# Kernel optimization log

Hardware: AMD Instinct MI355X
Metric: run time of the kernel (lower is better)

The kernel has to match this reference:

```python
import jax, jax.numpy as jnp
import numpy as np

N_EMBED = 384
N_HEADS = 8
HEAD_SIZE = N_EMBED // N_HEADS  # 48
BLOCK = 64
LN_EPS = 1e-5


def _layernorm(x, g, b):
    mu = jnp.mean(x, axis=-1, keepdims=True)
    var = jnp.var(x, axis=-1, keepdims=True)
    return (x - mu) * jax.lax.rsqrt(var + LN_EPS) * g + b


def setup_inputs() -> dict:
    key = jax.random.key(0)
    ks = jax.random.split(key, 16)
    s = 0.02
    x = jax.random.normal(ks[0], (2048, BLOCK, N_EMBED), dtype=jnp.float32)
    # per-head Q/K/V linears, stacked over heads (equivalent to the 8 separate nn.Linear's)
    wq = jax.random.normal(ks[1], (N_HEADS, N_EMBED, HEAD_SIZE), dtype=jnp.float32) * s
    bq = jnp.zeros((N_HEADS, HEAD_SIZE), dtype=jnp.float32)
    wk = jax.random.normal(ks[2], (N_HEADS, N_EMBED, HEAD_SIZE), dtype=jnp.float32) * s
    bk = jnp.zeros((N_HEADS, HEAD_SIZE), dtype=jnp.float32)
    wv = jax.random.normal(ks[3], (N_HEADS, N_EMBED, HEAD_SIZE), dtype=jnp.float32) * s
    bv = jnp.zeros((N_HEADS, HEAD_SIZE), dtype=jnp.float32)
    wo = jax.random.normal(ks[4], (N_EMBED, N_EMBED), dtype=jnp.float32) * s
    bo = jnp.zeros((N_EMBED,), dtype=jnp.float32)
    w1 = jax.random.normal(ks[5], (N_EMBED, 4 * N_EMBED), dtype=jnp.float32) * s
    b1 = jnp.zeros((4 * N_EMBED,), dtype=jnp.float32)
    w2 = jax.random.normal(ks[6], (4 * N_EMBED, N_EMBED), dtype=jnp.float32) * s
    b2 = jnp.zeros((N_EMBED,), dtype=jnp.float32)
    g1 = jnp.ones((N_EMBED,), dtype=jnp.float32)
    be1 = jnp.zeros((N_EMBED,), dtype=jnp.float32)
    g2 = jnp.ones((N_EMBED,), dtype=jnp.float32)
    be2 = jnp.zeros((N_EMBED,), dtype=jnp.float32)
    return dict(x=x, wq=wq, bq=bq, wk=wk, bk=bk, wv=wv, bv=bv, wo=wo, bo=bo,
                w1=w1, b1=b1, w2=w2, b2=b2, g1=g1, be1=be1, g2=g2, be2=be2)


def reference(x, wq, bq, wk, bk, wv, bv, wo, bo, w1, b1, w2, b2, g1, be1, g2, be2):
    B, T, D = x.shape  # T == BLOCK
    # x = norm1(x)
    h = _layernorm(x, g1, be1)
    # multi-head causal attention (heads stacked; same math as 8 separate SelfAttention modules)
    q = jnp.einsum('btd,hde->bhte', h, wq) + bq[None, :, None, :]
    k = jnp.einsum('btd,hde->bhte', h, wk) + bk[None, :, None, :]
    v = jnp.einsum('btd,hde->bhte', h, wv) + bv[None, :, None, :]
    scores = jnp.einsum('bhte,bhse->bhts', q, k) * (HEAD_SIZE ** -0.5)
    causal = jnp.tril(jnp.ones((T, T), dtype=bool))
    scores = jnp.where(causal, scores, -jnp.inf)
    probs = jax.nn.softmax(scores, axis=-1)  # dropout is identity in eval
    attn = jnp.einsum('bhts,bhse->bhte', probs, v)
    attn = attn.transpose(0, 2, 1, 3).reshape(B, T, N_HEADS * HEAD_SIZE)  # concat heads
    attn = attn @ wo + bo
    # x = x + attn(x)  (residual from the normed x, per the original code)
    h = h + attn
    # x = norm2(x); x = x + ff(x)
    h2 = _layernorm(h, g2, be2)
    ff = jax.nn.relu(h2 @ w1 + b1) @ w2 + b2
    return h2 + ff
```

## Files before the change

kernel.cpp:

```cpp
#include <hip/hip_runtime.h>

typedef __attribute__((ext_vector_type(8))) short short8;
typedef __attribute__((ext_vector_type(4))) float f32x4;

#define LNE 1e-5f

__device__ __forceinline__ unsigned short f2bf(float f) {
  union { float f; unsigned int u; } v; v.f = f;
  unsigned int r = v.u + 0x7fffu + ((v.u >> 16) & 1u);
  return (unsigned short)(r >> 16);
}
__device__ __forceinline__ float bf2f(unsigned short s) {
  union { unsigned int u; float f; } v; v.u = ((unsigned int)s) << 16;
  return v.f;
}
__device__ __forceinline__ unsigned int pk2(float a, float b) {
  return (unsigned int)f2bf(a) | ((unsigned int)f2bf(b) << 16);
}
__device__ __forceinline__ short8 ld8(const unsigned short* p, int k) {
  return *(const short8*)(p + k * 32);
}

__global__ void prep_kernel(const float* __restrict__ wq, const float* __restrict__ wk,
                            const float* __restrict__ wv, const float* __restrict__ wo,
                            const float* __restrict__ w1, const float* __restrict__ w2,
                            unsigned short* __restrict__ ws) {
  int idx = blockIdx.x * 256 + threadIdx.x;
  if (idx < 442368) {
    int n = idx / 384, d = idx % 384;
    int mat = n / 384, rem = n % 384, head = rem / 48, e = rem % 48;
    const float* w = (mat == 0) ? wq : ((mat == 1) ? wk : wv);
    ws[idx] = f2bf(w[(head * 384 + d) * 48 + e]);
  } else if (idx < 589824) {
    int j = idx - 442368; int n = j / 384, d = j % 384;
    ws[idx] = f2bf(wo[d * 384 + n]);
  } else if (idx < 1179648) {
    int j = idx - 589824; int n = j / 384, d = j % 384;
    ws[idx] = f2bf(w1[d * 1536 + n]);
  } else if (idx < 1769472) {
    int j = idx - 1179648; int n = j / 1536, c = j % 1536;
    ws[idx] = f2bf(w2[c * 384 + n]);
  }
}

__global__ __launch_bounds__(512, 2) void block_fused(
    const float* __restrict__ x,
    const float* __restrict__ bq, const float* __restrict__ bk, const float* __restrict__ bv,
    const float* __restrict__ bo, const float* __restrict__ b1, const float* __restrict__ b2,
    const float* __restrict__ g1, const float* __restrict__ be1,
    const float* __restrict__ g2, const float* __restrict__ be2,
    const unsigned short* __restrict__ wt,
    float* __restrict__ out) {
  __shared__ __align__(16) unsigned short sH[64 * 392];
  __shared__ __align__(16) unsigned short sA[64 * 392];
  __shared__ __align__(16) unsigned short sS[25344];

  const int tid  = threadIdx.x;
  const int wave = tid >> 6, lane = tid & 63;
  const int quad = lane >> 4, l15 = lane & 15;
  const int g = wave >> 2, w4 = wave & 3;
  const int b = blockIdx.x;

  const unsigned short* wqkvT = wt;
  const unsigned short* woT   = wt + 442368;
  const unsigned short* w1T   = wt + 589824;
  const unsigned short* w2T   = wt + 1179648;

  unsigned short* sQg = sS + g * 4608;
  unsigned short* sKg = sS + 9216 + g * 4608;
  unsigned short* sVg = sS + 18432 + g * 3456;

  {
    {
      int set = tid >> 8, j = tid & 255;
      int r = j >> 2, cc = 48 + (j & 3) * 4;
      *(uint2*)&sS[set * 4608 + r * 72 + cc] = make_uint2(0, 0);
      *(uint2*)&sS[9216 + set * 4608 + r * 72 + cc] = make_uint2(0, 0);
    }
    const int r = tid >> 3, sub = tid & 7;
    const float* xr = x + ((size_t)b * 64 + r) * 384 + sub * 48;
    float s = 0.f, s2 = 0.f;
#pragma unroll
    for (int i = 0; i < 12; ++i) {
      float4 v = ((const float4*)xr)[i];
      s  += v.x + v.y + v.z + v.w;
      s2 += v.x * v.x + v.y * v.y + v.z * v.z + v.w * v.w;
    }
    s  += __shfl_xor(s, 1);  s  += __shfl_xor(s, 2);  s  += __shfl_xor(s, 4);
    s2 += __shfl_xor(s2, 1); s2 += __shfl_xor(s2, 2); s2 += __shfl_xor(s2, 4);
    float mu = s * (1.f / 384.f);
    float rstd = rsqrtf(s2 * (1.f / 384.f) - mu * mu + LNE);
#pragma unroll
    for (int i = 0; i < 12; ++i) {
      float4 v = ((const float4*)xr)[i];
      int c = sub * 48 + i * 4;
      float h0 = (v.x - mu) * rstd * g1[c + 0] + be1[c + 0];
      float h1 = (v.y - mu) * rstd * g1[c + 1] + be1[c + 1];
      float h2 = (v.z - mu) * rstd * g1[c + 2] + be1[c + 2];
      float h3 = (v.w - mu) * rstd * g1[c + 3] + be1[c + 3];
      *(uint2*)&sH[r * 392 + c] = make_uint2(pk2(h0, h1), pk2(h2, h3));
    }
  }
  __syncthreads();

#pragma unroll 1
  for (int hp = 0; hp < 4; ++hp) {
    const int h = hp * 2 + g;
    if (hp) {
      int set = tid >> 8, j = tid & 255;
      int r = j >> 2, cc = 48 + (j & 3) * 4;
      *(uint2*)&sS[set * 4608 + r * 72 + cc] = make_uint2(0, 0);
    }
    {
      const int s0m = w4 / 3, s0e = w4 % 3;
      const int s1m = (w4 + 4) / 3, s1e = (w4 + 4) % 3;
      const bool has2 = (w4 == g);
      const unsigned short* bp0 = wqkvT + ((size_t)(s0m * 8 + h) * 48 + s0e * 16 + l15) * 384 + quad * 8;
      const unsigned short* bp1 = wqkvT + ((size_t)(s1m * 8 + h) * 48 + s1e * 16 + l15) * 384 + quad * 8;
      const unsigned short* bp2 = wqkvT + ((size_t)(16 + h) * 48 + 32 + l15) * 384 + quad * 8;
      const unsigned short* abase = sH + l15 * 392 + quad * 8;

      f32x4 acc0[4], acc1[4], acc2[4];
#pragma unroll
      for (int mt = 0; mt < 4; ++mt) {
        acc0[mt] = (f32x4){0.f, 0.f, 0.f, 0.f};
        acc1[mt] = (f32x4){0.f, 0.f, 0.f, 0.f};
        acc2[mt] = (f32x4){0.f, 0.f, 0.f, 0.f};
      }
      short8 b0[4], b1[4], b2[4];
#pragma unroll
      for (int k = 0; k < 3; ++k) {
        b0[k] = ld8(bp0, k); b1[k] = ld8(bp1, k);
        if (has2) b2[k] = ld8(bp2, k);
      }
#pragma unroll
      for (int k = 0; k < 12; ++k) {
        if (k < 9) {
          int sl = (k + 3) & 3;
          b0[sl] = ld8(bp0, k + 3); b1[sl] = ld8(bp1, k + 3);
          if (has2) b2[sl] = ld8(bp2, k + 3);
        }
        short8 a[4];
#pragma unroll
        for (int mt = 0; mt < 4; ++mt) a[mt] = *(const short8*)(abase + mt * 16 * 392 + k * 32);
        int sl = k & 3;
#pragma unroll
        for (int mt = 0; mt < 4; ++mt)
          acc0[mt] = __builtin_amdgcn_mfma_f32_16x16x32_bf16(a[mt], b0[sl], acc0[mt], 0, 0, 0);
#pragma unroll
        for (int mt = 0; mt < 4; ++mt)
          acc1[mt] = __builtin_amdgcn_mfma_f32_16x16x32_bf16(a[mt], b1[sl], acc1[mt], 0, 0, 0);
        if (has2) {
#pragma unroll
          for (int mt = 0; mt < 4; ++mt)
            acc2[mt] = __builtin_amdgcn_mfma_f32_16x16x32_bf16(a[mt], b2[sl], acc2[mt], 0, 0, 0);
        }
      }
      auto wrQKV = [&](int mat, int et, f32x4* acc) {
        const float* bias = (mat == 0) ? bq : ((mat == 1) ? bk : bv);
        float bsv = bias[h * 48 + et * 16 + l15];
        if (mat == 2) {
#pragma unroll
          for (int mt = 0; mt < 4; ++mt)
            *(uint2*)&sVg[(et * 16 + l15) * 72 + mt * 16 + quad * 4] =
                make_uint2(pk2(acc[mt][0] + bsv, acc[mt][1] + bsv),
                           pk2(acc[mt][2] + bsv, acc[mt][3] + bsv));
        } else {
          unsigned short* dst = (mat == 0) ? sQg : sKg;
#pragma unroll
          for (int mt = 0; mt < 4; ++mt)
#pragma unroll
            for (int i = 0; i < 4; ++i)
              dst[(mt * 16 + quad * 4 + i) * 72 + et * 16 + l15] = f2bf(acc[mt][i] + bsv);
        }
      };
      wrQKV(s0m, s0e, acc0);
      wrQKV(s1m, s1e, acc1);
      if (has2) wrQKV(2, 2, acc2);
    }
    __syncthreads();

    f32x4 sc[4];
#pragma unroll
    for (int ts = 0; ts < 4; ++ts) {
      f32x4 acc = {0.f, 0.f, 0.f, 0.f};
#pragma unroll
      for (int k = 0; k < 2; ++k) {
        short8 a  = *(const short8*)&sQg[(w4 * 16 + l15) * 72 + k * 32 + quad * 8];
        short8 bb = *(const short8*)&sKg[(ts * 16 + l15) * 72 + k * 32 + quad * 8];
        acc = __builtin_amdgcn_mfma_f32_16x16x32_bf16(a, bb, acc, 0, 0, 0);
      }
      sc[ts] = acc;
    }
    const float scale = 0.14433756729740645f;
#pragma unroll
    for (int i = 0; i < 4; ++i) {
      int t = w4 * 16 + quad * 4 + i;
      float vv[4];
#pragma unroll
      for (int ts = 0; ts < 4; ++ts) {
        int s_ = ts * 16 + l15;
        float v = sc[ts][i] * scale;
        vv[ts] = (s_ <= t) ? v : -INFINITY;
      }
      float mx = fmaxf(fmaxf(vv[0], vv[1]), fmaxf(vv[2], vv[3]));
      mx = fmaxf(mx, __shfl_xor(mx, 1)); mx = fmaxf(mx, __shfl_xor(mx, 2));
      mx = fmaxf(mx, __shfl_xor(mx, 4)); mx = fmaxf(mx, __shfl_xor(mx, 8));
      float sum = 0.f;
#pragma unroll
      for (int ts = 0; ts < 4; ++ts) { vv[ts] = __expf(vv[ts] - mx); sum += vv[ts]; }
      sum += __shfl_xor(sum, 1); sum += __shfl_xor(sum, 2);
      sum += __shfl_xor(sum, 4); sum += __shfl_xor(sum, 8);
      float inv = 1.f / sum;
#pragma unroll
      for (int ts = 0; ts < 4; ++ts)
        sQg[t * 72 + ts * 16 + l15] = f2bf(vv[ts] * inv);
    }
#pragma unroll
    for (int et = 0; et < 3; ++et) {
      f32x4 acc = {0.f, 0.f, 0.f, 0.f};
#pragma unroll
      for (int k = 0; k < 2; ++k) {
        short8 a  = *(const short8*)&sVg[(et * 16 + l15) * 72 + k * 32 + quad * 8];
        short8 bb = *(const short8*)&sQg[(w4 * 16 + l15) * 72 + k * 32 + quad * 8];
        acc = __builtin_amdgcn_mfma_f32_16x16x32_bf16(a, bb, acc, 0, 0, 0);
      }
      *(uint2*)&sA[(w4 * 16 + l15) * 392 + h * 48 + et * 16 + quad * 4] =
          make_uint2(pk2(acc[0], acc[1]), pk2(acc[2], acc[3]));
    }
    __syncthreads();
  }

  {
    float* sRedS  = (float*)sS;
    float* sRedS2 = (float*)sS + 512;
    const unsigned short* bp[3];
#pragma unroll
    for (int nl = 0; nl < 3; ++nl)
      bp[nl] = woT + (size_t)((wave * 3 + nl) * 16 + l15) * 384 + quad * 8;
    f32x4 oacc[3][4];
#pragma unroll
    for (int nl = 0; nl < 3; ++nl)
#pragma unroll
      for (int mt = 0; mt < 4; ++mt) oacc[nl][mt] = (f32x4){0.f, 0.f, 0.f, 0.f};
    short8 bb[3][4];
#pragma unroll
    for (int k = 0; k < 3; ++k)
#pragma unroll
      for (int nl = 0; nl < 3; ++nl) bb[nl][k] = ld8(bp[nl], k);
#pragma unroll
    for (int k = 0; k < 12; ++k) {
      if (k < 9) {
        int sl = (k + 3) & 3;
#pragma unroll
        for (int nl = 0; nl < 3; ++nl) bb[nl][sl] = ld8(bp[nl], k + 3);
      }
      short8 a[4];
#pragma unroll
      for (int mt = 0; mt < 4; ++mt)
        a[mt] = *(const short8*)&sA[(mt * 16 + l15) * 392 + k * 32 + quad * 8];
      int sl = k & 3;
#pragma unroll
      for (int nl = 0; nl < 3; ++nl)
#pragma unroll
        for (int mt = 0; mt < 4; ++mt)
          oacc[nl][mt] = __builtin_amdgcn_mfma_f32_16x16x32_bf16(a[mt], bb[nl][sl], oacc[nl][mt], 0, 0, 0);
    }
#pragma unroll
    for (int nl = 0; nl < 3; ++nl) {
      int n = (wave * 3 + nl) * 16 + l15;
      float bov = bo[n];
#pragma unroll
      for (int mt = 0; mt < 4; ++mt)
#pragma unroll
        for (int i = 0; i < 4; ++i)
          oacc[nl][mt][i] += bov + bf2f(sH[(mt * 16 + quad * 4 + i) * 392 + n]);
    }
#pragma unroll
    for (int mt = 0; mt < 4; ++mt)
#pragma unroll
      for (int i = 0; i < 4; ++i) {
        float s = oacc[0][mt][i] + oacc[1][mt][i] + oacc[2][mt][i];
        float s2 = oacc[0][mt][i] * oacc[0][mt][i] + oacc[1][mt][i] * oacc[1][mt][i]
                 + oacc[2][mt][i] * oacc[2][mt][i];
        s  += __shfl_xor(s, 1);  s  += __shfl_xor(s, 2);  s  += __shfl_xor(s, 4);  s  += __shfl_xor(s, 8);
        s2 += __shfl_xor(s2, 1); s2 += __shfl_xor(s2, 2); s2 += __shfl_xor(s2, 4); s2 += __shfl_xor(s2, 8);
        if (l15 == 0) {
          int row = mt * 16 + quad * 4 + i;
          sRedS[row * 8 + wave] = s;
          sRedS2[row * 8 + wave] = s2;
        }
      }
    __syncthreads();
    float mu_[4][4], rs_[4][4];
#pragma unroll
    for (int mt = 0; mt < 4; ++mt)
#pragma unroll
      for (int i = 0; i < 4; ++i) {
        int row = mt * 16 + quad * 4 + i;
        float4 p0 = *(float4*)&sRedS[row * 8], p1 = *(float4*)&sRedS[row * 8 + 4];
        float4 q0 = *(float4*)&sRedS2[row * 8], q1 = *(float4*)&sRedS2[row * 8 + 4];
        float st  = p0.x + p0.y + p0.z + p0.w + p1.x + p1.y + p1.z + p1.w;
        float s2t = q0.x + q0.y + q0.z + q0.w + q1.x + q1.y + q1.z + q1.w;
        float mu = st * (1.f / 384.f);
        mu_[mt][i] = mu;
        rs_[mt][i] = rsqrtf(s2t * (1.f / 384.f) - mu * mu + LNE);
      }
#pragma unroll
    for (int nl = 0; nl < 3; ++nl) {
      int n = (wave * 3 + nl) * 16 + l15;
      float gv = g2[n], bev = be2[n];
#pragma unroll
      for (int mt = 0; mt < 4; ++mt)
#pragma unroll
        for (int i = 0; i < 4; ++i) {
          float h2v = (oacc[nl][mt][i] - mu_[mt][i]) * rs_[mt][i] * gv + bev;
          sH[(mt * 16 + quad * 4 + i) * 392 + n] = f2bf(h2v);
        }
    }
  }
  __syncthreads();

  f32x4 facc[4][3];
#pragma unroll
  for (int mt = 0; mt < 4; ++mt)
#pragma unroll
    for (int nl = 0; nl < 3; ++nl) facc[mt][nl] = (f32x4){0.f, 0.f, 0.f, 0.f};

  auto FFN1 = [&](int c, unsigned short* U) {
    const unsigned short* ap[3];
#pragma unroll
    for (int ml = 0; ml < 3; ++ml)
      ap[ml] = w1T + (size_t)(c * 384 + (wave * 3 + ml) * 16 + l15) * 384 + quad * 8;
    f32x4 acc[3][4];
#pragma unroll
    for (int ml = 0; ml < 3; ++ml)
#pragma unroll
      for (int nt = 0; nt < 4; ++nt) acc[ml][nt] = (f32x4){0.f, 0.f, 0.f, 0.f};
    short8 av[3][4];
#pragma unroll
    for (int k = 0; k < 3; ++k)
#pragma unroll
      for (int ml = 0; ml < 3; ++ml) av[ml][k] = ld8(ap[ml], k);
#pragma unroll
    for (int k = 0; k < 12; ++k) {
      if (k < 9) {
        int sl = (k + 3) & 3;
#pragma unroll
        for (int ml = 0; ml < 3; ++ml) av[ml][sl] = ld8(ap[ml], k + 3);
      }
      short8 bb[4];
#pragma unroll
      for (int nt = 0; nt < 4; ++nt)
        bb[nt] = *(const short8*)&sH[(nt * 16 + l15) * 392 + k * 32 + quad * 8];
      int sl = k & 3;
#pragma unroll
      for (int ml = 0; ml < 3; ++ml)
#pragma unroll
        for (int nt = 0; nt < 4; ++nt)
          acc[ml][nt] = __builtin_amdgcn_mfma_f32_16x16x32_bf16(av[ml][sl], bb[nt], acc[ml][nt], 0, 0, 0);
    }
#pragma unroll
    for (int ml = 0; ml < 3; ++ml) {
      int mt = wave * 3 + ml;
      int rbase = c * 384 + mt * 16 + quad * 4;
#pragma unroll
      for (int nt = 0; nt < 4; ++nt) {
        float u0 = fmaxf(acc[ml][nt][0] + b1[rbase + 0], 0.f);
        float u1 = fmaxf(acc[ml][nt][1] + b1[rbase + 1], 0.f);
        float u2 = fmaxf(acc[ml][nt][2] + b1[rbase + 2], 0.f);
        float u3 = fmaxf(acc[ml][nt][3] + b1[rbase + 3], 0.f);
        *(uint2*)&U[(nt * 16 + l15) * 392 + mt * 16 + quad * 4] =
            make_uint2(pk2(u0, u1), pk2(u2, u3));
      }
    }
  };
  auto FFN2 = [&](int c, const unsigned short* U) {
    const unsigned short* bp[3];
#pragma unroll
    for (int nl = 0; nl < 3; ++nl)
      bp[nl] = w2T + (size_t)((wave * 3 + nl) * 16 + l15) * 1536 + c * 384 + quad * 8;
    short8 bb[3][4];
#pragma unroll
    for (int k = 0; k < 3; ++k)
#pragma unroll
      for (int nl = 0; nl < 3; ++nl) bb[nl][k] = ld8(bp[nl], k);
#pragma unroll
    for (int k = 0; k < 12; ++k) {
      if (k < 9) {
        int sl = (k + 3) & 3;
#pragma unroll
        for (int nl = 0; nl < 3; ++nl) bb[nl][sl] = ld8(bp[nl], k + 3);
      }
      short8 a[4];
#pragma unroll
      for (int mt = 0; mt < 4; ++mt)
        a[mt] = *(const short8*)&U[(mt * 16 + l15) * 392 + k * 32 + quad * 8];
      int sl = k & 3;
#pragma unroll
      for (int nl = 0; nl < 3; ++nl)
#pragma unroll
        for (int mt = 0; mt < 4; ++mt)
          facc[mt][nl] = __builtin_amdgcn_mfma_f32_16x16x32_bf16(a[mt], bb[nl][sl], facc[mt][nl], 0, 0, 0);
    }
  };

  FFN1(0, sA);
  __syncthreads();
#pragma unroll 1
  for (int c = 0; c < 4; ++c) {
    if (c < 3) FFN1(c + 1, (c & 1) ? sA : sS);
    FFN2(c, (c & 1) ? sS : sA);
    __syncthreads();
  }

#pragma unroll
  for (int nl = 0; nl < 3; ++nl) {
    int n = (wave * 3 + nl) * 16 + l15;
    float b2v = b2[n];
#pragma unroll
    for (int mt = 0; mt < 4; ++mt) {
#pragma unroll
      for (int i = 0; i < 4; ++i) {
        int t = mt * 16 + quad * 4 + i;
        float v = facc[mt][nl][i] + b2v + bf2f(sH[t * 392 + n]);
        out[((size_t)b * 64 + t) * 384 + n] = v;
      }
    }
  }
}

extern "C" void kernel_launch(void* const* d_in, const int* in_sizes, int n_in,
                              void* d_out, int out_size, void* d_ws, size_t ws_size,
                              hipStream_t stream) {
  const float* x   = (const float*)d_in[0];
  const float* wq  = (const float*)d_in[1];
  const float* bq  = (const float*)d_in[2];
  const float* wk  = (const float*)d_in[3];
  const float* bk  = (const float*)d_in[4];
  const float* wv  = (const float*)d_in[5];
  const float* bv  = (const float*)d_in[6];
  const float* wo  = (const float*)d_in[7];
  const float* bo  = (const float*)d_in[8];
  const float* w1  = (const float*)d_in[9];
  const float* b1  = (const float*)d_in[10];
  const float* w2  = (const float*)d_in[11];
  const float* b2  = (const float*)d_in[12];
  const float* g1  = (const float*)d_in[13];
  const float* be1 = (const float*)d_in[14];
  const float* g2  = (const float*)d_in[15];
  const float* be2 = (const float*)d_in[16];
  unsigned short* wt = (unsigned short*)d_ws;
  float* out = (float*)d_out;

  int nbatch = in_sizes[0] / (64 * 384);
  prep_kernel<<<(1769472 + 255) / 256, 256, 0, stream>>>(wq, wk, wv, wo, w1, w2, wt);
  block_fused<<<nbatch, 512, 0, stream>>>(x, bq, bk, bv, bo, b1, b2,
                                          g1, be1, g2, be2, wt, out);
}
```

Measured before the change: 1.341 ms.

## Prefetch next-stage weight fragments across barriers and use LDS-only barriers

Splits each GEMM stage into a prefetch part, which issues the first global weight loads, and a run part. The prefetch for the next head pair, for Wo, and for the next FFN chunk is issued before the barrier, so global latency overlaps synchronisation. __syncthreads is replaced by a barrier that waits only on LDS counters, so outstanding global loads can stay in flight across it. The V-projection work is rebalanced: every wave now computes one 16x16 V tile instead of two waves computing four, which evens the per-wave MFMA load. The cost is more live registers for the prefetch buffers, which may lower occupancy.

```diff
diff --git a/kernel.cpp b/kernel.cpp
--- a/kernel.cpp
+++ b/kernel.cpp
@@ -19,6 +19,12 @@
 }
 __device__ __forceinline__ short8 ld8(const unsigned short* p, int k) {
   return *(const short8*)(p + k * 32);
+}
+
+__device__ __forceinline__ void bar_lds() {
+  asm volatile("s_waitcnt lgkmcnt(0)" ::: "memory");
+  __builtin_amdgcn_s_barrier();
+  __builtin_amdgcn_sched_barrier(0);
 }
 
 __global__ void prep_kernel(const float* __restrict__ wq, const float* __restrict__ wk,
@@ -70,6 +76,75 @@
   unsigned short* sKg = sS + 9216 + g * 4608;
   unsigned short* sVg = sS + 18432 + g * 3456;
 
+  const unsigned short* qp0; const unsigned short* qp1; const unsigned short* qp2;
+  short8 qb0[4], qb1[4], qb2[4];
+  const int s0 = w4, s1 = w4 + 4;
+  const int m0 = s0 / 3, e0 = s0 % 3;
+  const int m1 = s1 / 3, e1 = s1 % 3;
+  auto QKV_PRE = [&](int h) {
+    qp0 = wqkvT + ((size_t)(m0 * 8 + h) * 48 + e0 * 16 + l15) * 384 + quad * 8;
+    qp1 = wqkvT + ((size_t)(m1 * 8 + h) * 48 + e1 * 16 + l15) * 384 + quad * 8;
+    qp2 = wqkvT + ((size_t)(16 + h) * 48 + 32 + l15) * 384 + quad * 8;
+#pragma unroll
+    for (int k = 0; k < 3; ++k) { qb0[k] = ld8(qp0, k); qb1[k] = ld8(qp1, k); qb2[k] = ld8(qp2, k); }
+  };
+  auto QKV_RUN = [&](int h) {
+    f32x4 acc0[4], acc1[4], acc2 = (f32x4){0.f, 0.f, 0.f, 0.f};
+#pragma unroll
+    for (int mt = 0; mt < 4; ++mt) {
+      acc0[mt] = (f32x4){0.f, 0.f, 0.f, 0.f};
+      acc1[mt] = (f32x4){0.f, 0.f, 0.f, 0.f};
+    }
+    const unsigned short* abase  = sH + l15 * 392 + quad * 8;
+    const unsigned short* abase2 = sH + (w4 * 16 + l15) * 392 + quad * 8;
+#pragma unroll
+    for (int k = 0; k < 12; ++k) {
+      if (k < 9) {
+        int sl = (k + 3) & 3;
+        qb0[sl] = ld8(qp0, k + 3); qb1[sl] = ld8(qp1, k + 3); qb2[sl] = ld8(qp2, k + 3);
+      }
+      short8 a[4];
+#pragma unroll
+      for (int mt = 0; mt < 4; ++mt) a[mt] = *(const short8*)(abase + mt * 16 * 392 + k * 32);
+      short8 a2 = *(const short8*)(abase2 + k * 32);
+      int sl = k & 3;
+#pragma unroll
+      for (int mt = 0; mt < 4; ++mt)
+        acc0[mt] = __builtin_amdgcn_mfma_f32_16x16x32_bf16(a[mt], qb0[sl], acc0[mt], 0, 0, 0);
+#pragma unroll
+      for (int mt = 0; mt < 4; ++mt)
+        acc1[mt] = __builtin_amdgcn_mfma_f32_16x16x32_bf16(a[mt], qb1[sl], acc1[mt], 0, 0, 0);
+      acc2 = __builtin_amdgcn_mfma_f32_16x16x32_bf16(a2, qb2[sl], acc2, 0, 0, 0);
+    }
+    auto wrStream = [&](int m, int e, f32x4* acc) {
+      const float* bias = (m == 0) ? bq : ((m == 1) ? bk : bv);
+      float bsv = bias[h * 48 + e * 16 + l15];
+      if (m == 2) {
+#pragma unroll
+        for (int mt = 0; mt < 4; ++mt)
+          *(uint2*)&sVg[(e * 16 + l15) * 72 + mt * 16 + quad * 4] =
+              make_uint2(pk2(acc[mt][0] + bsv, acc[mt][1] + bsv),
+                         pk2(acc[mt][2] + bsv, acc[mt][3] + bsv));
+      } else {
+        unsigned short* dst = (m == 0) ? sQg : sKg;
+#pragma unroll
+        for (int mt = 0; mt < 4; ++mt)
+#pragma unroll
+          for (int i = 0; i < 4; ++i)
+            dst[(mt * 16 + quad * 4 + i) * 72 + e * 16 + l15] = f2bf(acc[mt][i] + bsv);
+      }
+    };
+    wrStream(m0, e0, acc0);
+    wrStream(m1, e1, acc1);
+    {
+      float bsv = bv[h * 48 + 32 + l15];
+      *(uint2*)&sVg[(32 + l15) * 72 + w4 * 16 + quad * 4] =
+          make_uint2(pk2(acc2[0] + bsv, acc2[1] + bsv), pk2(acc2[2] + bsv, acc2[3] + bsv));
+    }
+  };
+
+  const unsigned short* obp[3]; short8 ob[3][4];
+
   {
     {
       int set = tid >> 8, j = tid & 255;
@@ -101,7 +176,8 @@
       *(uint2*)&sH[r * 392 + c] = make_uint2(pk2(h0, h1), pk2(h2, h3));
     }
   }
-  __syncthreads();
+  QKV_PRE(g);
+  bar_lds();
 
 #pragma unroll 1
   for (int hp = 0; hp < 4; ++hp) {
@@ -111,74 +187,18 @@
       int r = j >> 2, cc = 48 + (j & 3) * 4;
       *(uint2*)&sS[set * 4608 + r * 72 + cc] = make_uint2(0, 0);
     }
-    {
-      const int s0m = w4 / 3, s0e = w4 % 3;
-      const int s1m = (w4 + 4) / 3, s1e = (w4 + 4) % 3;
-      const bool has2 = (w4 == g);
-      const unsigned short* bp0 = wqkvT + ((size_t)(s0m * 8 + h) * 48 + s0e * 16 + l15) * 384 + quad * 8;
-      const unsigned short* bp1 = wqkvT + ((size_t)(s1m * 8 + h) * 48 + s1e * 16 + l15) * 384 + quad * 8;
-      const unsigned short* bp2 = wqkvT + ((size_t)(16 + h) * 48 + 32 + l15) * 384 + quad * 8;
-      const unsigned short* abase = sH + l15 * 392 + quad * 8;
-
-      f32x4 acc0[4], acc1[4], acc2[4];
-#pragma unroll
-      for (int mt = 0; mt < 4; ++mt) {
-        acc0[mt] = (f32x4){0.f, 0.f, 0.f, 0.f};
-        acc1[mt] = (f32x4){0.f, 0.f, 0.f, 0.f};
-        acc2[mt] = (f32x4){0.f, 0.f, 0.f, 0.f};
-      }
-      short8 b0[4], b1[4], b2[4];
-#pragma unroll
-      for (int k = 0; k < 3; ++k) {
-        b0[k] = ld8(bp0, k); b1[k] = ld8(bp1, k);
-        if (has2) b2[k] = ld8(bp2, k);
-      }
-#pragma unroll
-      for (int k = 0; k < 12; ++k) {
-        if (k < 9) {
-          int sl = (k + 3) & 3;
-          b0[sl] = ld8(bp0, k + 3); b1[sl] = ld8(bp1, k + 3);
-          if (has2) b2[sl] = ld8(bp2, k + 3);
-        }
-        short8 a[4];
-#pragma unroll
-        for (int mt = 0; mt < 4; ++mt) a[mt] = *(const short8*)(abase + mt * 16 * 392 + k * 32);
-        int sl = k & 3;
-#pragma unroll
-        for (int mt = 0; mt < 4; ++mt)
-          acc0[mt] = __builtin_amdgcn_mfma_f32_16x16x32_bf16(a[mt], b0[sl], acc0[mt], 0, 0, 0);
-#pragma unroll
-        for (int mt = 0; mt < 4; ++mt)
-          acc1[mt] = __builtin_amdgcn_mfma_f32_16x16x32_bf16(a[mt], b1[sl], acc1[mt], 0, 0, 0);
-        if (has2) {
-#pragma unroll
-          for (int mt = 0; mt < 4; ++mt)
-            acc2[mt] = __builtin_amdgcn_mfma_f32_16x16x32_bf16(a[mt], b2[sl], acc2[mt], 0, 0, 0);
-        }
-      }
-      auto wrQKV = [&](int mat, int et, f32x4* acc) {
-        const float* bias = (mat == 0) ? bq : ((mat == 1) ? bk : bv);
-        float bsv = bias[h * 48 + et * 16 + l15];
-        if (mat == 2) {
-#pragma unroll
-          for (int mt = 0; mt < 4; ++mt)
-            *(uint2*)&sVg[(et * 16 + l15) * 72 + mt * 16 + quad * 4] =
-                make_uint2(pk2(acc[mt][0] + bsv, acc[mt][1] + bsv),
-                           pk2(acc[mt][2] + bsv, acc[mt][3] + bsv));
-        } else {
-          unsigned short* dst = (mat == 0) ? sQg : sKg;
-#pragma unroll
-          for (int mt = 0; mt < 4; ++mt)
-#pragma unroll
-            for (int i = 0; i < 4; ++i)
-              dst[(mt * 16 + quad * 4 + i) * 72 + et * 16 + l15] = f2bf(acc[mt][i] + bsv);
-        }
-      };
-      wrQKV(s0m, s0e, acc0);
-      wrQKV(s1m, s1e, acc1);
-      if (has2) wrQKV(2, 2, acc2);
-    }
-    __syncthreads();
+    QKV_RUN(h);
+    if (hp < 3) QKV_PRE(h + 2);
+    bar_lds();
+
+    if (hp == 3) {
+#pragma unroll
+      for (int nl = 0; nl < 3; ++nl) {
+        obp[nl] = woT + (size_t)((wave * 3 + nl) * 16 + l15) * 384 + quad * 8;
+#pragma unroll
+        for (int k = 0; k < 3; ++k) ob[nl][k] = ld8(obp[nl], k);
+      }
+    }
 
     f32x4 sc[4];
 #pragma unroll
@@ -228,32 +248,106 @@
       *(uint2*)&sA[(w4 * 16 + l15) * 392 + h * 48 + et * 16 + quad * 4] =
           make_uint2(pk2(acc[0], acc[1]), pk2(acc[2], acc[3]));
     }
-    __syncthreads();
-  }
+    bar_lds();
+  }
+
+  const unsigned short* f1p[3]; short8 f1a[3][4];
+  const unsigned short* f2p[3]; short8 f2b[3][4];
+  auto F1_PRE = [&](int c) {
+#pragma unroll
+    for (int ml = 0; ml < 3; ++ml) {
+      f1p[ml] = w1T + (size_t)(c * 384 + (wave * 3 + ml) * 16 + l15) * 384 + quad * 8;
+#pragma unroll
+      for (int k = 0; k < 3; ++k) f1a[ml][k] = ld8(f1p[ml], k);
+    }
+  };
+  auto F1_RUN = [&](int c, unsigned short* U) {
+    f32x4 acc[3][4];
+#pragma unroll
+    for (int ml = 0; ml < 3; ++ml)
+#pragma unroll
+      for (int nt = 0; nt < 4; ++nt) acc[ml][nt] = (f32x4){0.f, 0.f, 0.f, 0.f};
+#pragma unroll
+    for (int k = 0; k < 12; ++k) {
+      if (k < 9) {
+        int sl = (k + 3) & 3;
+#pragma unroll
+        for (int ml = 0; ml < 3; ++ml) f1a[ml][sl] = ld8(f1p[ml], k + 3);
+      }
+      short8 bb[4];
+#pragma unroll
+      for (int nt = 0; nt < 4; ++nt)
+        bb[nt] = *(const short8*)&sH[(nt * 16 + l15) * 392 + k * 32 + quad * 8];
+      int sl = k & 3;
+#pragma unroll
+      for (int ml = 0; ml < 3; ++ml)
+#pragma unroll
+        for (int nt = 0; nt < 4; ++nt)
+          acc[ml][nt] = __builtin_amdgcn_mfma_f32_16x16x32_bf16(f1a[ml][sl], bb[nt], acc[ml][nt], 0, 0, 0);
+    }
+#pragma unroll
+    for (int ml = 0; ml < 3; ++ml) {
+      int mt = wave * 3 + ml;
+      int rbase = c * 384 + mt * 16 + quad * 4;
+#pragma unroll
+      for (int nt = 0; nt < 4; ++nt) {
+        float u0 = fmaxf(acc[ml][nt][0] + b1[rbase + 0], 0.f);
+        float u1 = fmaxf(acc[ml][nt][1] + b1[rbase + 1], 0.f);
+        float u2 = fmaxf(acc[ml][nt][2] + b1[rbase + 2], 0.f);
+        float u3 = fmaxf(acc[ml][nt][3] + b1[rbase + 3], 0.f);
+        *(uint2*)&U[(nt * 16 + l15) * 392 + mt * 16 + quad * 4] =
+            make_uint2(pk2(u0, u1), pk2(u2, u3));
+      }
+    }
+  };
+  f32x4 facc[4][3];
+#pragma unroll
+  for (int mt = 0; mt < 4; ++mt)
+#pragma unroll
+    for (int nl = 0; nl < 3; ++nl) facc[mt][nl] = (f32x4){0.f, 0.f, 0.f, 0.f};
+  auto F2_PRE = [&](int c) {
+#pragma unroll
+    for (int nl = 0; nl < 3; ++nl) {
+      f2p[nl] = w2T + (size_t)((wave * 3 + nl) * 16 + l15) * 1536 + c * 384 + quad * 8;
+#pragma unroll
+      for (int k = 0; k < 3; ++k) f2b[nl][k] = ld8(f2p[nl], k);
+    }
+  };
+  auto F2_RUN = [&](int c, const unsigned short* U) {
+#pragma unroll
+    for (int k = 0; k < 12; ++k) {
+      if (k < 9) {
+        int sl = (k + 3) & 3;
+#pragma unroll
+        for (int nl = 0; nl < 3; ++nl) f2b[nl][sl] = ld8(f2p[nl], k + 3);
+      }
+      short8 a[4];
+#pragma unroll
+      for (int mt = 0; mt < 4; ++mt)
+        a[mt] = *(const short8*)&U[(mt * 16 + l15) * 392 + k * 32 + quad * 8];
+      int sl = k & 3;
+#pragma unroll
+      for (int nl = 0; nl < 3; ++nl)
+#pragma unroll
+        for (int mt = 0; mt < 4; ++mt)
+          facc[mt][nl] = __builtin_amdgcn_mfma_f32_16x16x32_bf16(a[mt], f2b[nl][sl], facc[mt][nl], 0, 0, 0);
+    }
+  };
 
   {
     float* sRedS  = (float*)sS;
     float* sRedS2 = (float*)sS + 512;
-    const unsigned short* bp[3];
+    f32x4 oacc[3][4];
 #pragma unroll
     for (int nl = 0; nl < 3; ++nl)
-      bp[nl] = woT + (size_t)((wave * 3 + nl) * 16 + l15) * 384 + quad * 8;
-    f32x4 oacc[3][4];
-#pragma unroll
-    for (int nl = 0; nl < 3; ++nl)
 #pragma unroll
       for (int mt = 0; mt < 4; ++mt) oacc[nl][mt] = (f32x4){0.f, 0.f, 0.f, 0.f};
-    short8 bb[3][4];
-#pragma unroll
-    for (int k = 0; k < 3; ++k)
-#pragma unroll
-      for (int nl = 0; nl < 3; ++nl) bb[nl][k] = ld8(bp[nl], k);
 #pragma unroll
     for (int k = 0; k < 12; ++k) {
       if (k < 9) {
         int sl = (k + 3) & 3;
 #pragma unroll
-        for (int nl = 0; nl < 3; ++nl) bb[nl][sl] = ld8(bp[nl], k + 3);
+        for (int nl = 0; nl < 3; ++nl) ob[nl][sl] = ld8(obp[nl], k + 3);
       }
       short8 a[4];
 #pragma unroll
@@ -264,7 +358,7 @@
       for (int nl = 0; nl < 3; ++nl)
 #pragma unroll
         for (int mt = 0; mt < 4; ++mt)
-          oacc[nl][mt] = __builtin_amdgcn_mfma_f32_16x16x32_bf16(a[mt], bb[nl][sl], oacc[nl][mt], 0, 0, 0);
+          oacc[nl][mt] = __builtin_amdgcn_mfma_f32_16x16x32_bf16(a[mt], ob[nl][sl], oacc[nl][mt], 0, 0, 0);
     }
 #pragma unroll
     for (int nl = 0; nl < 3; ++nl) {
@@ -291,7 +385,7 @@
           sRedS2[row * 8 + wave] = s2;
         }
       }
-    __syncthreads();
+    bar_lds();
     float mu_[4][4], rs_[4][4];
 #pragma unroll
     for (int mt = 0; mt < 4; ++mt)
@@ -319,99 +413,22 @@
         }
     }
   }
-  __syncthreads();
-
-  f32x4 facc[4][3];
-#pragma unroll
-  for (int mt = 0; mt < 4; ++mt)
-#pragma unroll
-    for (int nl = 0; nl < 3; ++nl) facc[mt][nl] = (f32x4){0.f, 0.f, 0.f, 0.f};
-
-  auto FFN1 = [&](int c, unsigned short* U) {
-    const unsigned short* ap[3];
-#pragma unroll
-    for (int ml = 0; ml < 3; ++ml)
-      ap[ml] = w1T + (size_t)(c * 384 + (wave * 3 + ml) * 16 + l15) * 384 + quad * 8;
-    f32x4 acc[3][4];
-#pragma unroll
-    for (int ml = 0; ml < 3; ++ml)
-#pragma unroll
-      for (int nt = 0; nt < 4; ++nt) acc[ml][nt] = (f32x4){0.f, 0.f, 0.f, 0.f};
-    short8 av[3][4];
-#pragma unroll
-    for (int k = 0; k < 3; ++k)
-#pragma unroll
-      for (int ml = 0; ml < 3; ++ml) av[ml][k] = ld8(ap[ml], k);
-#pragma unroll
-    for (int k = 0; k < 12; ++k) {
-      if (k < 9) {
-        int sl = (k + 3) & 3;
-#pragma unroll
-        for (int ml = 0; ml < 3; ++ml) av[ml][sl] = ld8(ap[ml], k + 3);
-      }
-      short8 bb[4];
-#pragma unroll
-      for (int nt = 0; nt < 4; ++nt)
-        bb[nt] = *(const short8*)&sH[(nt * 16 + l15) * 392 + k * 32 + quad * 8];
-      int sl = k & 3;
-#pragma unroll
-      for (int ml = 0; ml < 3; ++ml)
-#pragma unroll
-        for (int nt = 0; nt < 4; ++nt)
-          acc[ml][nt] = __builtin_amdgcn_mfma_f32_16x16x32_bf16(av[ml][sl], bb[nt], acc[ml][nt], 0, 0, 0);
-    }
-#pragma unroll
-    for (int ml = 0; ml < 3; ++ml) {
-      int mt = wave * 3 + ml;
-      int rbase = c * 384 + mt * 16 + quad * 4;
-#pragma unroll
-      for (int nt = 0; nt < 4; ++nt) {
-        float u0 = fmaxf(acc[ml][nt][0] + b1[rbase + 0], 0.f);
-        float u1 = fmaxf(acc[ml][nt][1] + b1[rbase + 1], 0.f);
-        float u2 = fmaxf(acc[ml][nt][2] + b1[rbase + 2], 0.f);
-        float u3 = fmaxf(acc[ml][nt][3] + b1[rbase + 3], 0.f);
-        *(uint2*)&U[(nt * 16 + l15) * 392 + mt * 16 + quad * 4] =
-            make_uint2(pk2(u0, u1), pk2(u2, u3));
-      }
-    }
-  };
-  auto FFN2 = [&](int c, const unsigned short* U) {
-    const unsigned short* bp[3];
-#pragma unroll
-    for (int nl = 0; nl < 3; ++nl)
-      bp[nl] = w2T + (size_t)((wave * 3 + nl) * 16 + l15) * 1536 + c * 384 + quad * 8;
-    short8 bb[3][4];
-#pragma unroll
-    for (int k = 0; k < 3; ++k)
-#pragma unroll
-      for (int nl = 0; nl < 3; ++nl) bb[nl][k] = ld8(bp[nl], k);
-#pragma unroll
-    for (int k = 0; k < 12; ++k) {
-      if (k < 9) {
-        int sl = (k + 3) & 3;
-#pragma unroll
-        for (int nl = 0; nl < 3; ++nl) bb[nl][sl] = ld8(bp[nl], k + 3);
-      }
-      short8 a[4];
-#pragma unroll
-      for (int mt = 0; mt < 4; ++mt)
-        a[mt] = *(const short8*)&U[(mt * 16 + l15) * 392 + k * 32 + quad * 8];
-      int sl = k & 3;
-#pragma unroll
-      for (int nl = 0; nl < 3; ++nl)
-#pragma unroll
-        for (int mt = 0; mt < 4; ++mt)
-          facc[mt][nl] = __builtin_amdgcn_mfma_f32_16x16x32_bf16(a[mt], bb[nl][sl], facc[mt][nl], 0, 0, 0);
-    }
-  };
-
-  FFN1(0, sA);
-  __syncthreads();
+  F1_PRE(0);
+  bar_lds();
+
+  F1_RUN(0, sA);
+  F2_PRE(0);
+  F1_PRE(1);
+  bar_lds();
 #pragma unroll 1
   for (int c = 0; c < 4; ++c) {
-    if (c < 3) FFN1(c + 1, (c & 1) ? sA : sS);
-    FFN2(c, (c & 1) ? sS : sA);
-    __syncthreads();
+    if (c < 3) F1_RUN(c + 1, (c & 1) ? sA : sS);
+    F2_RUN(c, (c & 1) ? sS : sA);
+    if (c < 3) {
+      F2_PRE(c + 1);
+      if (c < 2) F1_PRE(c + 2);
+      bar_lds();
+    }
   }
 
 #pragma unroll
```

New measurement: 1.386 ms. 3.4% more time.
